# Kernel tuning notes

Measured on AMD Instinct MI355X. Metric: run time of the kernel, lower is better.

## Reference

```python
import jax, jax.numpy as jnp
import numpy as np

STATE_DIM = 8
SLOT_DIM = 128
B, T, K = 128, 6, 64


def _mlp(x, w1, b1, w2, b2):
    return jax.nn.relu(x @ w1 + b1) @ w2 + b2


def setup_inputs() -> dict:
    key = jax.random.key(0)
    ks = jax.random.split(key, 24)
    s = 0.02
    def w(k, shape):
        return jax.random.normal(k, shape, dtype=jnp.float32) * s
    D, H = STATE_DIM, SLOT_DIM
    return {
        "gt_states": jax.random.normal(ks[0], (B, T, K, D), dtype=jnp.float32),
        "rollout_steps": 5,
        "enc_w1": w(ks[1], (D, H)),  "enc_b1": jnp.zeros((H,), jnp.float32),
        "enc_w2": w(ks[2], (H, H)),  "enc_b2": jnp.zeros((H,), jnp.float32),
        "self_w1": w(ks[3], (H, H)), "self_b1": jnp.zeros((H,), jnp.float32),
        "self_w2": w(ks[4], (H, H)), "self_b2": jnp.zeros((H,), jnp.float32),
        "inter_w1": w(ks[5], (2 * H, H)), "inter_b1": jnp.zeros((H,), jnp.float32),
        "inter_w2": w(ks[6], (H, H)),     "inter_b2": jnp.zeros((H,), jnp.float32),
        "upd_w1": w(ks[7], (2 * H, H)), "upd_b1": jnp.zeros((H,), jnp.float32),
        "upd_w2": w(ks[8], (H, H)),     "upd_b2": jnp.zeros((H,), jnp.float32),
        "dec_w1": w(ks[9], (H, H)),  "dec_b1": jnp.zeros((H,), jnp.float32),
        "dec_w2": w(ks[10], (H, D)), "dec_b2": jnp.zeros((D,), jnp.float32),
    }


def reference(gt_states, rollout_steps, enc_w1, enc_b1, enc_w2, enc_b2,
              self_w1, self_b1, self_w2, self_b2,
              inter_w1, inter_b1, inter_w2, inter_b2,
              upd_w1, upd_b1, upd_w2, upd_b2,
              dec_w1, dec_b1, dec_w2, dec_b2):
    Tn = gt_states.shape[1]
    n_steps = min(Tn - 1, int(rollout_steps))
    H = enc_w1.shape[1]
    # split the concat-MLP first layer: cat([si, sj]) @ W1 == si @ W1a + sj @ W1b
    wi_a, wi_b = inter_w1[:H], inter_w1[H:]

    slots = _mlp(gt_states[:, 0], enc_w1, enc_b1, enc_w2, enc_b2)  # [B,K,H]
    preds = []
    for _ in range(n_steps):
        delta_self = _mlp(slots, self_w1, self_b1, self_w2, self_b2)  # [B,K,H]
        a = slots @ wi_a  # sender (i) contribution, [B,K,H]
        b = slots @ wi_b  # receiver (j) contribution, [B,K,H]
        # pairwise pre-activation [B,K(i),K(j),H]
        pre = a[:, :, None, :] + b[:, None, :, :] + inter_b1
        effects = jax.nn.relu(pre) @ inter_w2 + inter_b2  # [B,K,K,H]
        delta_inter = effects.mean(axis=1)  # mean over i -> [B,K,H]
        slots = _mlp(jnp.concatenate([delta_self, delta_inter], axis=-1),
                     upd_w1, upd_b1, upd_w2, upd_b2)
        pred = _mlp(slots, dec_w1, dec_b1, dec_w2, dec_b2)  # [B,K,D]
        preds.append(pred)
        slots = _mlp(pred, enc_w1, enc_b1, enc_w2, enc_b2)
    pred_states = jnp.stack(preds, axis=1)  # [B,n_steps,K,D]
    target_states = gt_states[:, 1:int(rollout_steps) + 1]
    return pred_states, target_states
```

## Files before the change

kernel.cpp:

```cpp
#include <hip/hip_runtime.h>

#define BB 128
#define TT 6
#define KK 64
#define DD 8
#define HH 128
#define NSTEP 5
#define LDP 136
#define PREDSZ (BB*NSTEP*KK*DD)

typedef unsigned short u16;
typedef unsigned int   u32;
typedef _Float16 f16;
typedef __attribute__((ext_vector_type(8))) _Float16 f16x8;
typedef __attribute__((ext_vector_type(4))) float f32x4;
typedef __attribute__((ext_vector_type(2))) unsigned int u32x2;
typedef __attribute__((ext_vector_type(4))) unsigned int u32x4;
typedef __attribute__((ext_vector_type(2))) _Float16 h2;

union h2u { u32 u; h2 h; };
union hu  { u16 u; f16 h; };

__device__ __forceinline__ u16 f2h_bits(float f){
  hu v; v.h = (f16)f; return v.u;
}
__device__ __forceinline__ u32 pk2(float x, float y){
  hu a, b; a.h = (f16)x; b.h = (f16)y;
  return (u32)a.u | ((u32)b.u << 16);
}
__device__ __forceinline__ h2 u2h(u32 x){ h2u t; t.u = x; return t.h; }
__device__ __forceinline__ u32 h2u_(h2 x){ h2u t; t.h = x; return t.u; }

#define O_EWA   0
#define O_EWB   16384
#define O_EWS   32768
#define O_SUIU  49152
#define O_UD    81920
#define O_DET   98304
#define O_DW2T  114688
#define BIASF   57856
#define O_XBUF  131072
#define O_FLAG  (O_XBUF + 128*2*2*4096)

template<bool RELU>
__device__ __forceinline__ void gemmH(const u16 (*A)[LDP], const u16* __restrict__ wt,
    float bias, u16 (*O)[LDP], int wn, int l15, int q, int n, int lane)
{
  f16x8 bf[4];
#pragma unroll
  for (int kc=0; kc<4; ++kc)
    bf[kc] = *(const f16x8*)(wt + (wn<<11) + (kc<<9) + (lane<<3));
#pragma unroll
  for (int mt=0; mt<2; ++mt){
    f32x4 acc = {0.f,0.f,0.f,0.f};
#pragma unroll
    for (int kc=0; kc<4; ++kc){
      f16x8 af = *(const f16x8*)&A[(mt<<4)+l15][(kc<<5)+(q<<3)];
      acc = __builtin_amdgcn_mfma_f32_16x16x32_f16(af, bf[kc], acc, 0,0,0);
    }
#pragma unroll
    for (int e=0; e<4; ++e){
      float v = acc[e] + bias;
      if (RELU) v = fmaxf(v, 0.f);
      O[(mt<<4)+(q<<2)+e][n] = f2h_bits(v);
    }
  }
}

__device__ __forceinline__ void gemm256H(const u16 (*A1)[LDP], const u16 (*A2)[LDP],
    const u16* __restrict__ wt, float bias, u16 (*O)[LDP], int wn, int l15, int q, int n, int lane)
{
  f16x8 bf[8];
#pragma unroll
  for (int kc=0; kc<8; ++kc)
    bf[kc] = *(const f16x8*)(wt + (wn<<12) + (kc<<9) + (lane<<3));
#pragma unroll
  for (int mt=0; mt<2; ++mt){
    f32x4 acc = {0.f,0.f,0.f,0.f};
#pragma unroll
    for (int kc=0; kc<8; ++kc){
      const u16 (*As)[LDP] = (kc<4) ? A1 : A2;
      f16x8 af = *(const f16x8*)&As[(mt<<4)+l15][((kc&3)<<5)+(q<<3)];
      acc = __builtin_amdgcn_mfma_f32_16x16x32_f16(af, bf[kc], acc, 0,0,0);
    }
#pragma unroll
    for (int e=0; e<4; ++e){
      float v = fmaxf(acc[e] + bias, 0.f);
      O[(mt<<4)+(q<<2)+e][n] = f2h_bits(v);
    }
  }
}

__device__ __forceinline__ void fusedS1I(const u16 (*P)[LDP], const u16* __restrict__ ws,
    float bAv, float bBv, float bSv,
    u16 (*Q)[LDP], u16 (*S)[LDP],
    int wn, int half, int l15, int q, int n, int lane)
{
  f16x8 fa[4], fb[4], fs[4];
#pragma unroll
  for (int kc=0; kc<4; ++kc){
    const int o = (wn<<11) + (kc<<9) + (lane<<3);
    fa[kc] = *(const f16x8*)(ws + O_EWA + o);
    fb[kc] = *(const f16x8*)(ws + O_EWB + o);
    fs[kc] = *(const f16x8*)(ws + O_EWS + o);
  }
  u32 aPk[4][2], bPk[4][2];
#pragma unroll
  for (int mt=0; mt<4; ++mt){
    f16x8 af[4];
#pragma unroll
    for (int kc=0; kc<4; ++kc)
      af[kc] = *(const f16x8*)&P[(mt<<4)+l15][(kc<<5)+(q<<3)];
    f32x4 aA = {0.f,0.f,0.f,0.f}, aB = {0.f,0.f,0.f,0.f};
#pragma unroll
    for (int kc=0; kc<4; ++kc){
      aA = __builtin_amdgcn_mfma_f32_16x16x32_f16(af[kc], fa[kc], aA, 0,0,0);
      aB = __builtin_amdgcn_mfma_f32_16x16x32_f16(af[kc], fb[kc], aB, 0,0,0);
    }
    aPk[mt][0] = pk2(aA[0]+bAv, aA[1]+bAv);
    aPk[mt][1] = pk2(aA[2]+bAv, aA[3]+bAv);
    bPk[mt][0] = pk2(aB[0]+bBv, aB[1]+bBv);
    bPk[mt][1] = pk2(aB[2]+bBv, aB[3]+bBv);
    if ((mt>>1) == half){
      f32x4 hA = {0.f,0.f,0.f,0.f};
#pragma unroll
      for (int kc=0; kc<4; ++kc)
        hA = __builtin_amdgcn_mfma_f32_16x16x32_f16(af[kc], fs[kc], hA, 0,0,0);
#pragma unroll
      for (int e=0; e<4; ++e)
        S[((mt&1)<<4)+(q<<2)+e][n] = f2h_bits(fmaxf(hA[e]+bSv, 0.f));
    }
  }

  const u32 b0 = bPk[(half<<1)][0],   b1 = bPk[(half<<1)][1];
  const u32 b2 = bPk[(half<<1)+1][0], b3 = bPk[(half<<1)+1][1];
  u32 jt[4][4];
#pragma unroll
  for (int qp=0; qp<4; ++qp){
    const int src = (qp<<4) + l15;
    jt[qp][0] = (u32)__shfl((int)b0, src);
    jt[qp][1] = (u32)__shfl((int)b1, src);
    jt[qp][2] = (u32)__shfl((int)b2, src);
    jt[qp][3] = (u32)__shfl((int)b3, src);
  }
  h2 z; z.x = (f16)0.f; z.y = (f16)0.f;
  h2 s[4][4];
#pragma unroll
  for (int qp=0; qp<4; ++qp)
#pragma unroll
    for (int X=0; X<4; ++X) s[qp][X] = z;
#pragma unroll
  for (int mt=0; mt<4; ++mt)
#pragma unroll
    for (int p=0; p<2; ++p){
      const u32 ap = aPk[mt][p];
      const h2 hl = u2h(__builtin_amdgcn_perm(ap, ap, 0x01000100));
      const h2 hh = u2h(__builtin_amdgcn_perm(ap, ap, 0x03020302));
#pragma unroll
      for (int qp=0; qp<4; ++qp)
#pragma unroll
        for (int X=0; X<4; ++X){
          const h2 bt = u2h(jt[qp][X]);
          s[qp][X] += __builtin_elementwise_max(hl + bt, z);
          s[qp][X] += __builtin_elementwise_max(hh + bt, z);
        }
    }
#pragma unroll
  for (int m=0; m<2; ++m){
    const int msk = 16 << m;
#pragma unroll
    for (int qp=0; qp<4; ++qp)
#pragma unroll
      for (int X=0; X<4; ++X)
        s[qp][X] += u2h((u32)__shfl_xor((int)h2u_(s[qp][X]), msk));
  }
#pragma unroll
  for (int qp=0; qp<4; ++qp) if (qp == q){
#pragma unroll
    for (int X=0; X<4; ++X){
      const int mh = X>>1, p = X&1;
      const int j = (mh<<4) + (qp<<2) + (p<<1);
      hu lo, hi; lo.h = s[qp][X].x; hi.h = s[qp][X].y;
      Q[j][n]   = lo.u;
      Q[j+1][n] = hi.u;
    }
  }
}

__device__ __forceinline__ void dec_out(const u16 (*S)[LDP], const u16* __restrict__ dwt,
    float db2v, float* __restrict__ out, int batch, int half, int t, int tid)
{
  const int r = tid>>3, d = tid&7;
  float acc = db2v;
#pragma unroll
  for (int c=0; c<16; ++c){
    f16x8 hv = *(const f16x8*)&S[r][c<<3];
    f16x8 wv = *(const f16x8*)(dwt + (d<<7) + (c<<3));
#pragma unroll
    for (int j=0; j<8; ++j)
      acc += (float)hv[j] * (float)wv[j];
  }
  out[(size_t)(batch*NSTEP + t)*(KK*DD) + ((half<<5)+r)*DD + d] = acc;
}

__device__ __forceinline__ void mlp_in8(const float* pred, const float* __restrict__ W,
    const float* __restrict__ bias, u16 (*O)[LDP], int tid)
{
  const int h = tid & 127, rg = tid >> 7;
  float wv[DD];
#pragma unroll
  for (int d=0; d<DD; ++d) wv[d] = W[d*HH + h];
  const float bv = bias[h];
  for (int rr=0; rr<16; ++rr){
    const int r = (rg<<4) + rr;
    float v = bv;
#pragma unroll
    for (int d=0; d<DD; ++d) v += pred[r*DD + d] * wv[d];
    O[r][h] = f2h_bits(fmaxf(v, 0.f));
  }
}

__global__ void prep_kernel(
    const float* __restrict__ ew1, const float* __restrict__ eb1,
    const float* __restrict__ ew2, const float* __restrict__ eb2,
    const float* __restrict__ sw1, const float* __restrict__ sb1,
    const float* __restrict__ sw2, const float* __restrict__ sb2,
    const float* __restrict__ iw1, const float* __restrict__ ib1,
    const float* __restrict__ iw2, const float* __restrict__ ib2,
    const float* __restrict__ uw1, const float* __restrict__ ub1,
    const float* __restrict__ uw2, const float* __restrict__ ub2,
    const float* __restrict__ dw1, const float* __restrict__ db1,
    const float* __restrict__ dw2, const float* __restrict__ db2,
    u16* __restrict__ ws)
{
  const int idx = blockIdx.x * 256 + threadIdx.x;
  if (idx < 512) ((u32*)(ws + O_FLAG))[idx] = 0;
  if (idx < 49152){
    const int mat = idx >> 14, r = idx & 16383;
    const int g = r >> 11, kc = (r >> 9) & 3, lane = (r >> 3) & 63, e = r & 7;
    const int k  = (kc<<5) + ((lane>>4)<<3) + e;
    const int nn = (g<<4) + (lane & 15);
    float v = 0.f;
    if (mat == 0){ for (int m=0; m<HH; ++m) v += ew2[k*HH+m] * iw1[m*HH+nn]; }
    else if (mat == 1){ for (int m=0; m<HH; ++m) v += ew2[k*HH+m] * iw1[(HH+m)*HH+nn]; }
    else { for (int m=0; m<HH; ++m) v += ew2[k*HH+m] * sw1[m*HH+nn]; }
    hu hb; hb.h = (f16)v; ws[idx] = hb.u;
  } else if (idx < 81920){
    const int r = idx - 49152;
    const int g = r >> 12, kc = (r >> 9) & 7, lane = (r >> 3) & 63, e = r & 7;
    const int k  = ((kc&3)<<5) + ((lane>>4)<<3) + e;
    const int nn = (g<<4) + (lane & 15);
    float v = 0.f;
    if (kc < 4){ for (int m=0; m<HH; ++m) v += sw2[k*HH+m] * uw1[m*HH+nn]; }
    else { for (int m=0; m<HH; ++m) v += iw2[k*HH+m] * uw1[(HH+m)*HH+nn]; v *= (1.f/64.f); }
    hu hb; hb.h = (f16)v; ws[idx] = hb.u;
  } else if (idx < 98304){
    const int r = idx - 81920;
    const int g = r >> 11, kc = (r >> 9) & 3, lane = (r >> 3) & 63, e = r & 7;
    const int k  = (kc<<5) + ((lane>>4)<<3) + e;
    const int nn = (g<<4) + (lane & 15);
    float v = 0.f;
    for (int m=0; m<HH; ++m) v += uw2[k*HH+m] * dw1[m*HH+nn];
    hu hb; hb.h = (f16)v; ws[idx] = hb.u;
  } else if (idx < 114688){
    const int r = idx - 98304;
    const int g = r >> 11, kc = (r >> 9) & 3, lane = (r >> 3) & 63, e = r & 7;
    const int k  = (kc<<5) + ((lane>>4)<<3) + e;
    const int nn = (g<<4) + (lane & 15);
    float v = 0.f;
#pragma unroll
    for (int d=0; d<DD; ++d) v += dw2[k*DD+d] * ew1[d*HH+nn];
    hu hb; hb.h = (f16)v; ws[idx] = hb.u;
  } else if (idx < 115712){
    const int r = idx - 114688, d = r >> 7, hcol = r & 127;
    hu hb; hb.h = (f16)dw2[hcol*DD + d]; ws[idx] = hb.u;
  } else if (idx < 116480){
    const int j = idx - 115712, which = j >> 7, nn = j & 127;
    float v = 0.f;
    switch (which){
      case 0: for (int m=0; m<HH; ++m) v += eb2[m] * iw1[m*HH+nn]; break;
      case 1: for (int m=0; m<HH; ++m) v += eb2[m] * iw1[(HH+m)*HH+nn]; v += ib1[nn]; break;
      case 2: for (int m=0; m<HH; ++m) v += eb2[m] * sw1[m*HH+nn]; v += sb1[nn]; break;
      case 3: for (int m=0; m<HH; ++m) v += sb2[m]*uw1[m*HH+nn] + ib2[m]*uw1[(HH+m)*HH+nn];
              v += ub1[nn]; break;
      case 4: for (int m=0; m<HH; ++m) v += ub2[m] * dw1[m*HH+nn]; v += db1[nn]; break;
      default:
#pragma unroll
        for (int d=0; d<DD; ++d) v += db2[d] * ew1[d*HH+nn];
        v += eb1[nn]; break;
    }
    ((float*)ws)[BIASF + j] = v;
  }
}

__global__ __launch_bounds__(512, 2) void rollout_kernel(
    const float* __restrict__ gt, const int* __restrict__ rollout,
    const float* __restrict__ ew1, const float* __restrict__ eb1,
    const float* __restrict__ db2,
    u16* __restrict__ ws, float* __restrict__ out)
{
  extern __shared__ u16 smem[];
  u16 (*P)[LDP] = (u16(*)[LDP])smem;
  u16 (*Q)[LDP] = (u16(*)[LDP])(smem + 64*LDP);
  u16 (*R)[LDP] = (u16(*)[LDP])(smem + 96*LDP);
  u16 (*S)[LDP] = (u16(*)[LDP])(smem + 128*LDP);
  float* predbuf = (float*)Q;

  const int tid = threadIdx.x, blk = blockIdx.x;
  const int batch = blk & 127, half = blk >> 7;
  const int w = tid >> 6, lane = tid & 63;
  const int l15 = lane & 15, q = lane >> 4;
  const int wn = w;
  const int n = (wn << 4) + l15;

  int ns = rollout[0];
  if (ns > TT-1) ns = TT-1;
  if (ns > NSTEP) ns = NSTEP;
  if (ns < 0) ns = 0;

  const float* bf32 = (const float*)ws;
  const float bAv  = bf32[BIASF + n];
  const float bBv  = bf32[BIASF + 128 + n];
  const float bSv  = bf32[BIASF + 256 + n];
  const float bUv  = bf32[BIASF + 384 + n];
  const float bUDv = bf32[BIASF + 512 + n];
  const float debv = bf32[BIASF + 640 + n];
  const float db2v = db2[tid & 7];

  u16* xbuf  = ws + O_XBUF;
  u32* flags = (u32*)(ws + O_FLAG);
  const int own  = (batch<<1) + half;
  const int prt  = (batch<<1) + (1-half);

  for (int i=tid; i<NSTEP*KK*DD/2; i+=512)
    out[PREDSZ + batch*(NSTEP*KK*DD) + half*(NSTEP*KK*DD/2) + i]
      = gt[(size_t)batch*(TT*KK*DD) + KK*DD + half*(NSTEP*KK*DD/2) + i];
  predbuf[tid] = gt[(size_t)batch*(TT*KK*DD) + tid];
  __syncthreads();
  mlp_in8(predbuf, ew1, eb1, P, tid);
  __syncthreads();

  for (int t=0; t<ns; ++t){
    fusedS1I(P, ws, bAv, bBv, bSv, Q, S, wn, half, l15, q, n, lane);
    __syncthreads();
    gemm256H(S, Q, ws+O_SUIU, bUv, R, wn, l15, q, n, lane);
    __syncthreads();
    gemmH<true>(R, ws+O_UD, bUDv, S, wn, l15, q, n, lane);
    __syncthreads();
    gemmH<true>(S, ws+O_DET, debv, P + (half<<5), wn, l15, q, n, lane);
    if (tid < 256) dec_out(S, ws+O_DW2T, db2v, out, batch, half, t, tid);
    __syncthreads();

    if (t < ns-1){
      const int par = t & 1;
      u16* ob = xbuf + (((own<<1)|par) << 12);
      {
        const int r = tid >> 4, c = (tid & 15) << 3;
        *(f16x8*)(ob + tid*8) = *(const f16x8*)&P[(half<<5)+r][c];
      }
      __syncthreads();
      if (tid == 0){
        __hip_atomic_store(&flags[(own<<1)|par], (u32)(t+1),
                           __ATOMIC_RELEASE, __HIP_MEMORY_SCOPE_AGENT);
        int guard = 0;
        while (__hip_atomic_load(&flags[(prt<<1)|par],
                 __ATOMIC_ACQUIRE, __HIP_MEMORY_SCOPE_AGENT) != (u32)(t+1)
               && guard < (1<<22)){
          ++guard;
          __builtin_amdgcn_s_sleep(1);
        }
      }
      __syncthreads();
      {
        const u16* pb = xbuf + (((prt<<1)|par) << 12);
        const int r = tid >> 4, c = (tid & 15) << 3;
        *(f16x8*)&P[((1-half)<<5)+r][c] = *(const f16x8*)(pb + tid*8);
      }
      __syncthreads();
    }
  }
}

extern "C" void kernel_launch(void* const* d_in, const int* in_sizes, int n_in,
                              void* d_out, int out_size, void* d_ws, size_t ws_size,
                              hipStream_t stream)
{
  const float* gt  = (const float*)d_in[0];
  const int*   rs  = (const int*)d_in[1];
  const float* ew1 = (const float*)d_in[2];
  const float* eb1 = (const float*)d_in[3];
  const float* ew2 = (const float*)d_in[4];
  const float* eb2 = (const float*)d_in[5];
  const float* sw1 = (const float*)d_in[6];
  const float* sb1 = (const float*)d_in[7];
  const float* sw2 = (const float*)d_in[8];
  const float* sb2 = (const float*)d_in[9];
  const float* iw1 = (const float*)d_in[10];
  const float* ib1 = (const float*)d_in[11];
  const float* iw2 = (const float*)d_in[12];
  const float* ib2 = (const float*)d_in[13];
  const float* uw1 = (const float*)d_in[14];
  const float* ub1 = (const float*)d_in[15];
  const float* uw2 = (const float*)d_in[16];
  const float* ub2 = (const float*)d_in[17];
  const float* dw1 = (const float*)d_in[18];
  const float* db1 = (const float*)d_in[19];
  const float* dw2 = (const float*)d_in[20];
  const float* db2 = (const float*)d_in[21];
  float* out = (float*)d_out;
  u16*   ws  = (u16*)d_ws;

  const int smem_bytes = 160 * LDP * (int)sizeof(u16);
  (void)hipFuncSetAttribute((const void*)rollout_kernel,
                            hipFuncAttributeMaxDynamicSharedMemorySize, smem_bytes);

  hipLaunchKernelGGL(prep_kernel, dim3(455), dim3(256), 0, stream,
                     ew1, eb1, ew2, eb2, sw1, sb1, sw2, sb2, iw1, ib1, iw2, ib2,
                     uw1, ub1, uw2, ub2, dw1, db1, dw2, db2, ws);
  hipLaunchKernelGGL(rollout_kernel, dim3(2*BB), dim3(512), smem_bytes, stream,
                     gt, rs, ew1, eb1, db2, ws, out);
}
```

Before: 198.3 us.

## Split each batch across four cooperating blocks instead of two

```diff
diff --git a/kernel.cpp b/kernel.cpp
--- a/kernel.cpp
+++ b/kernel.cpp
@@ -14,8 +14,6 @@
 typedef _Float16 f16;
 typedef __attribute__((ext_vector_type(8))) _Float16 f16x8;
 typedef __attribute__((ext_vector_type(4))) float f32x4;
-typedef __attribute__((ext_vector_type(2))) unsigned int u32x2;
-typedef __attribute__((ext_vector_type(4))) unsigned int u32x4;
 typedef __attribute__((ext_vector_type(2))) _Float16 h2;
 
 union h2u { u32 u; h2 h; };
@@ -40,129 +38,122 @@
 #define O_DW2T  114688
 #define BIASF   57856
 #define O_XBUF  131072
-#define O_FLAG  (O_XBUF + 128*2*2*4096)
+#define O_FLAG  (O_XBUF + 128*4*2*2048)
 
 template<bool RELU>
-__device__ __forceinline__ void gemmH(const u16 (*A)[LDP], const u16* __restrict__ wt,
+__device__ __forceinline__ void gemm16(const u16 (*A)[LDP], const u16* __restrict__ wt,
     float bias, u16 (*O)[LDP], int wn, int l15, int q, int n, int lane)
 {
   f16x8 bf[4];
 #pragma unroll
   for (int kc=0; kc<4; ++kc)
     bf[kc] = *(const f16x8*)(wt + (wn<<11) + (kc<<9) + (lane<<3));
-#pragma unroll
-  for (int mt=0; mt<2; ++mt){
-    f32x4 acc = {0.f,0.f,0.f,0.f};
-#pragma unroll
-    for (int kc=0; kc<4; ++kc){
-      f16x8 af = *(const f16x8*)&A[(mt<<4)+l15][(kc<<5)+(q<<3)];
-      acc = __builtin_amdgcn_mfma_f32_16x16x32_f16(af, bf[kc], acc, 0,0,0);
-    }
-#pragma unroll
-    for (int e=0; e<4; ++e){
-      float v = acc[e] + bias;
-      if (RELU) v = fmaxf(v, 0.f);
-      O[(mt<<4)+(q<<2)+e][n] = f2h_bits(v);
-    }
-  }
-}
-
-__device__ __forceinline__ void gemm256H(const u16 (*A1)[LDP], const u16 (*A2)[LDP],
+  f32x4 acc = {0.f,0.f,0.f,0.f};
+#pragma unroll
+  for (int kc=0; kc<4; ++kc){
+    f16x8 af = *(const f16x8*)&A[l15][(kc<<5)+(q<<3)];
+    acc = __builtin_amdgcn_mfma_f32_16x16x32_f16(af, bf[kc], acc, 0,0,0);
+  }
+#pragma unroll
+  for (int e=0; e<4; ++e){
+    float v = acc[e] + bias;
+    if (RELU) v = fmaxf(v, 0.f);
+    O[(q<<2)+e][n] = f2h_bits(v);
+  }
+}
+
+__device__ __forceinline__ void gemm256_16(const u16 (*A1)[LDP], const u16 (*A2)[LDP],
     const u16* __restrict__ wt, float bias, u16 (*O)[LDP], int wn, int l15, int q, int n, int lane)
 {
   f16x8 bf[8];
 #pragma unroll
   for (int kc=0; kc<8; ++kc)
     bf[kc] = *(const f16x8*)(wt + (wn<<12) + (kc<<9) + (lane<<3));
-#pragma unroll
-  for (int mt=0; mt<2; ++mt){
-    f32x4 acc = {0.f,0.f,0.f,0.f};
-#pragma unroll
-    for (int kc=0; kc<8; ++kc){
-      const u16 (*As)[LDP] = (kc<4) ? A1 : A2;
-      f16x8 af = *(const f16x8*)&As[(mt<<4)+l15][((kc&3)<<5)+(q<<3)];
-      acc = __builtin_amdgcn_mfma_f32_16x16x32_f16(af, bf[kc], acc, 0,0,0);
-    }
-#pragma unroll
-    for (int e=0; e<4; ++e){
-      float v = fmaxf(acc[e] + bias, 0.f);
-      O[(mt<<4)+(q<<2)+e][n] = f2h_bits(v);
-    }
+  f32x4 acc = {0.f,0.f,0.f,0.f};
+#pragma unroll
+  for (int kc=0; kc<8; ++kc){
+    const u16 (*As)[LDP] = (kc<4) ? A1 : A2;
+    f16x8 af = *(const f16x8*)&As[l15][((kc&3)<<5)+(q<<3)];
+    acc = __builtin_amdgcn_mfma_f32_16x16x32_f16(af, bf[kc], acc, 0,0,0);
+  }
+#pragma unroll
+  for (int e=0; e<4; ++e){
+    float v = fmaxf(acc[e] + bias, 0.f);
+    O[(q<<2)+e][n] = f2h_bits(v);
   }
 }
 
 __device__ __forceinline__ void fusedS1I(const u16 (*P)[LDP], const u16* __restrict__ ws,
     float bAv, float bBv, float bSv,
     u16 (*Q)[LDP], u16 (*S)[LDP],
-    int wn, int half, int l15, int q, int n, int lane)
-{
-  f16x8 fa[4], fb[4], fs[4];
-#pragma unroll
-  for (int kc=0; kc<4; ++kc){
-    const int o = (wn<<11) + (kc<<9) + (lane<<3);
-    fa[kc] = *(const f16x8*)(ws + O_EWA + o);
-    fb[kc] = *(const f16x8*)(ws + O_EWB + o);
-    fs[kc] = *(const f16x8*)(ws + O_EWS + o);
-  }
-  u32 aPk[4][2], bPk[4][2];
-#pragma unroll
-  for (int mt=0; mt<4; ++mt){
-    f16x8 af[4];
+    int wn, int qtr, int l15, int q, int n, int lane)
+{
+  u32 aPk[4][2];
+  {
+    f16x8 fa[4];
 #pragma unroll
     for (int kc=0; kc<4; ++kc)
-      af[kc] = *(const f16x8*)&P[(mt<<4)+l15][(kc<<5)+(q<<3)];
-    f32x4 aA = {0.f,0.f,0.f,0.f}, aB = {0.f,0.f,0.f,0.f};
+      fa[kc] = *(const f16x8*)(ws + O_EWA + (wn<<11) + (kc<<9) + (lane<<3));
+#pragma unroll
+    for (int mt=0; mt<4; ++mt){
+      f32x4 aA = {0.f,0.f,0.f,0.f};
+#pragma unroll
+      for (int kc=0; kc<4; ++kc){
+        f16x8 af = *(const f16x8*)&P[(mt<<4)+l15][(kc<<5)+(q<<3)];
+        aA = __builtin_amdgcn_mfma_f32_16x16x32_f16(af, fa[kc], aA, 0,0,0);
+      }
+      aPk[mt][0] = pk2(aA[0]+bAv, aA[1]+bAv);
+      aPk[mt][1] = pk2(aA[2]+bAv, aA[3]+bAv);
+    }
+  }
+  u32 bPk[2];
+  {
+    f16x8 fb[4], fs[4], af[4];
 #pragma unroll
     for (int kc=0; kc<4; ++kc){
-      aA = __builtin_amdgcn_mfma_f32_16x16x32_f16(af[kc], fa[kc], aA, 0,0,0);
+      const int o = (wn<<11) + (kc<<9) + (lane<<3);
+      fb[kc] = *(const f16x8*)(ws + O_EWB + o);
+      fs[kc] = *(const f16x8*)(ws + O_EWS + o);
+      af[kc] = *(const f16x8*)&P[(qtr<<4)+l15][(kc<<5)+(q<<3)];
+    }
+    f32x4 aB = {0.f,0.f,0.f,0.f}, aS = {0.f,0.f,0.f,0.f};
+#pragma unroll
+    for (int kc=0; kc<4; ++kc){
       aB = __builtin_amdgcn_mfma_f32_16x16x32_f16(af[kc], fb[kc], aB, 0,0,0);
-    }
-    aPk[mt][0] = pk2(aA[0]+bAv, aA[1]+bAv);
-    aPk[mt][1] = pk2(aA[2]+bAv, aA[3]+bAv);
-    bPk[mt][0] = pk2(aB[0]+bBv, aB[1]+bBv);
-    bPk[mt][1] = pk2(aB[2]+bBv, aB[3]+bBv);
-    if ((mt>>1) == half){
-      f32x4 hA = {0.f,0.f,0.f,0.f};
-#pragma unroll
-      for (int kc=0; kc<4; ++kc)
-        hA = __builtin_amdgcn_mfma_f32_16x16x32_f16(af[kc], fs[kc], hA, 0,0,0);
-#pragma unroll
-      for (int e=0; e<4; ++e)
-        S[((mt&1)<<4)+(q<<2)+e][n] = f2h_bits(fmaxf(hA[e]+bSv, 0.f));
-    }
-  }
-
-  const u32 b0 = bPk[(half<<1)][0],   b1 = bPk[(half<<1)][1];
-  const u32 b2 = bPk[(half<<1)+1][0], b3 = bPk[(half<<1)+1][1];
-  u32 jt[4][4];
+      aS = __builtin_amdgcn_mfma_f32_16x16x32_f16(af[kc], fs[kc], aS, 0,0,0);
+    }
+    bPk[0] = pk2(aB[0]+bBv, aB[1]+bBv);
+    bPk[1] = pk2(aB[2]+bBv, aB[3]+bBv);
+#pragma unroll
+    for (int e=0; e<4; ++e)
+      S[(q<<2)+e][n] = f2h_bits(fmaxf(aS[e]+bSv, 0.f));
+  }
+
+  u32 jt[4][2];
 #pragma unroll
   for (int qp=0; qp<4; ++qp){
     const int src = (qp<<4) + l15;
-    jt[qp][0] = (u32)__shfl((int)b0, src);
-    jt[qp][1] = (u32)__shfl((int)b1, src);
-    jt[qp][2] = (u32)__shfl((int)b2, src);
-    jt[qp][3] = (u32)__shfl((int)b3, src);
+    jt[qp][0] = (u32)__shfl((int)bPk[0], src);
+    jt[qp][1] = (u32)__shfl((int)bPk[1], src);
   }
   h2 z; z.x = (f16)0.f; z.y = (f16)0.f;
-  h2 s[4][4];
-#pragma unroll
-  for (int qp=0; qp<4; ++qp)
-#pragma unroll
-    for (int X=0; X<4; ++X) s[qp][X] = z;
+  h2 s[4][2];
+#pragma unroll
+  for (int qp=0; qp<4; ++qp){ s[qp][0] = z; s[qp][1] = z; }
 #pragma unroll
   for (int mt=0; mt<4; ++mt)
 #pragma unroll
-    for (int p=0; p<2; ++p){
-      const u32 ap = aPk[mt][p];
+    for (int pp=0; pp<2; ++pp){
+      const u32 ap = aPk[mt][pp];
       const h2 hl = u2h(__builtin_amdgcn_perm(ap, ap, 0x01000100));
       const h2 hh = u2h(__builtin_amdgcn_perm(ap, ap, 0x03020302));
 #pragma unroll
       for (int qp=0; qp<4; ++qp)
 #pragma unroll
-        for (int X=0; X<4; ++X){
-          const h2 bt = u2h(jt[qp][X]);
-          s[qp][X] += __builtin_elementwise_max(hl + bt, z);
-          s[qp][X] += __builtin_elementwise_max(hh + bt, z);
+        for (int p=0; p<2; ++p){
+          const h2 bt = u2h(jt[qp][p]);
+          s[qp][p] += __builtin_elementwise_max(hl + bt, z);
+          s[qp][p] += __builtin_elementwise_max(hh + bt, z);
         }
     }
 #pragma unroll
@@ -171,16 +162,15 @@
 #pragma unroll
     for (int qp=0; qp<4; ++qp)
 #pragma unroll
-      for (int X=0; X<4; ++X)
-        s[qp][X] += u2h((u32)__shfl_xor((int)h2u_(s[qp][X]), msk));
+      for (int p=0; p<2; ++p)
+        s[qp][p] += u2h((u32)__shfl_xor((int)h2u_(s[qp][p]), msk));
   }
 #pragma unroll
   for (int qp=0; qp<4; ++qp) if (qp == q){
 #pragma unroll
-    for (int X=0; X<4; ++X){
-      const int mh = X>>1, p = X&1;
-      const int j = (mh<<4) + (qp<<2) + (p<<1);
-      hu lo, hi; lo.h = s[qp][X].x; hi.h = s[qp][X].y;
+    for (int p=0; p<2; ++p){
+      const int j = (qp<<2) + (p<<1);
+      hu lo, hi; lo.h = s[qp][p].x; hi.h = s[qp][p].y;
       Q[j][n]   = lo.u;
       Q[j+1][n] = hi.u;
     }
@@ -188,7 +178,7 @@
 }
 
 __device__ __forceinline__ void dec_out(const u16 (*S)[LDP], const u16* __restrict__ dwt,
-    float db2v, float* __restrict__ out, int batch, int half, int t, int tid)
+    float db2v, float* __restrict__ out, int batch, int qtr, int t, int tid)
 {
   const int r = tid>>3, d = tid&7;
   float acc = db2v;
@@ -200,7 +190,7 @@
     for (int j=0; j<8; ++j)
       acc += (float)hv[j] * (float)wv[j];
   }
-  out[(size_t)(batch*NSTEP + t)*(KK*DD) + ((half<<5)+r)*DD + d] = acc;
+  out[(size_t)(batch*NSTEP + t)*(KK*DD) + ((qtr<<4)+r)*DD + d] = acc;
 }
 
 __device__ __forceinline__ void mlp_in8(const float* pred, const float* __restrict__ W,
@@ -234,7 +224,7 @@
     u16* __restrict__ ws)
 {
   const int idx = blockIdx.x * 256 + threadIdx.x;
-  if (idx < 512) ((u32*)(ws + O_FLAG))[idx] = 0;
+  if (idx < 1024) ((u32*)(ws + O_FLAG))[idx] = 0;
   if (idx < 49152){
     const int mat = idx >> 14, r = idx & 16383;
     const int g = r >> 11, kc = (r >> 9) & 3, lane = (r >> 3) & 63, e = r & 7;
@@ -302,12 +292,12 @@
   extern __shared__ u16 smem[];
   u16 (*P)[LDP] = (u16(*)[LDP])smem;
   u16 (*Q)[LDP] = (u16(*)[LDP])(smem + 64*LDP);
-  u16 (*R)[LDP] = (u16(*)[LDP])(smem + 96*LDP);
-  u16 (*S)[LDP] = (u16(*)[LDP])(smem + 128*LDP);
+  u16 (*R)[LDP] = (u16(*)[LDP])(smem + 80*LDP);
+  u16 (*S)[LDP] = (u16(*)[LDP])(smem + 96*LDP);
   float* predbuf = (float*)Q;
 
   const int tid = threadIdx.x, blk = blockIdx.x;
-  const int batch = blk & 127, half = blk >> 7;
+  const int batch = blk & 127, qtr = blk >> 7;
   const int w = tid >> 6, lane = tid & 63;
   const int l15 = lane & 15, q = lane >> 4;
   const int wn = w;
@@ -329,52 +319,70 @@
 
   u16* xbuf  = ws + O_XBUF;
   u32* flags = (u32*)(ws + O_FLAG);
-  const int own  = (batch<<1) + half;
-  const int prt  = (batch<<1) + (1-half);
-
-  for (int i=tid; i<NSTEP*KK*DD/2; i+=512)
-    out[PREDSZ + batch*(NSTEP*KK*DD) + half*(NSTEP*KK*DD/2) + i]
-      = gt[(size_t)batch*(TT*KK*DD) + KK*DD + half*(NSTEP*KK*DD/2) + i];
+
+  for (int i = tid; i < (NSTEP*KK*DD/4); i += 512)
+    out[PREDSZ + batch*(NSTEP*KK*DD) + qtr*(NSTEP*KK*DD/4) + i]
+      = gt[(size_t)batch*(TT*KK*DD) + KK*DD + qtr*(NSTEP*KK*DD/4) + i];
   predbuf[tid] = gt[(size_t)batch*(TT*KK*DD) + tid];
   __syncthreads();
   mlp_in8(predbuf, ew1, eb1, P, tid);
   __syncthreads();
 
   for (int t=0; t<ns; ++t){
-    fusedS1I(P, ws, bAv, bBv, bSv, Q, S, wn, half, l15, q, n, lane);
+    fusedS1I(P, ws, bAv, bBv, bSv, Q, S, wn, qtr, l15, q, n, lane);
     __syncthreads();
-    gemm256H(S, Q, ws+O_SUIU, bUv, R, wn, l15, q, n, lane);
+    gemm256_16(S, Q, ws+O_SUIU, bUv, R, wn, l15, q, n, lane);
     __syncthreads();
-    gemmH<true>(R, ws+O_UD, bUDv, S, wn, l15, q, n, lane);
+    gemm16<true>(R, ws+O_UD, bUDv, S, wn, l15, q, n, lane);
     __syncthreads();
-    gemmH<true>(S, ws+O_DET, debv, P + (half<<5), wn, l15, q, n, lane);
-    if (tid < 256) dec_out(S, ws+O_DW2T, db2v, out, batch, half, t, tid);
+    {
+      f16x8 bfw[4];
+#pragma unroll
+      for (int kc=0; kc<4; ++kc)
+        bfw[kc] = *(const f16x8*)(ws + O_DET + (wn<<11) + (kc<<9) + (lane<<3));
+      f32x4 acc = {0.f,0.f,0.f,0.f};
+#pragma unroll
+      for (int kc=0; kc<4; ++kc){
+        f16x8 af = *(const f16x8*)&S[l15][(kc<<5)+(q<<3)];
+        acc = __builtin_amdgcn_mfma_f32_16x16x32_f16(af, bfw[kc], acc, 0,0,0);
+      }
+      const int par = t & 1;
+      u16* ob = xbuf + ((((batch<<2)|qtr)<<1|par)<<11);
+      const bool exch = (t < ns-1);
+#pragma unroll
+      for (int e=0; e<4; ++e){
+        const u16 bits = f2h_bits(fmaxf(acc[e]+debv, 0.f));
+        P[(qtr<<4)+(q<<2)+e][n] = bits;
+        if (exch) ob[(((q<<2)+e)<<7) | n] = bits;
+      }
+    }
+    if (tid < 128) dec_out(S, ws+O_DW2T, db2v, out, batch, qtr, t, tid);
     __syncthreads();
 
     if (t < ns-1){
       const int par = t & 1;
-      u16* ob = xbuf + (((own<<1)|par) << 12);
-      {
-        const int r = tid >> 4, c = (tid & 15) << 3;
-        *(f16x8*)(ob + tid*8) = *(const f16x8*)&P[(half<<5)+r][c];
-      }
-      __syncthreads();
       if (tid == 0){
-        __hip_atomic_store(&flags[(own<<1)|par], (u32)(t+1),
+        __hip_atomic_store(&flags[((batch<<2)|qtr)<<1|par], (u32)(t+1),
                            __ATOMIC_RELEASE, __HIP_MEMORY_SCOPE_AGENT);
-        int guard = 0;
-        while (__hip_atomic_load(&flags[(prt<<1)|par],
-                 __ATOMIC_ACQUIRE, __HIP_MEMORY_SCOPE_AGENT) != (u32)(t+1)
-               && guard < (1<<22)){
-          ++guard;
-          __builtin_amdgcn_s_sleep(1);
+#pragma unroll
+        for (int qq=0; qq<4; ++qq) if (qq != qtr){
+          int guard = 0;
+          while (__hip_atomic_load(&flags[((batch<<2)|qq)<<1|par],
+                   __ATOMIC_ACQUIRE, __HIP_MEMORY_SCOPE_AGENT) != (u32)(t+1)
+                 && guard < (1<<22)){
+            ++guard;
+            __builtin_amdgcn_s_sleep(1);
+          }
         }
       }
       __syncthreads();
-      {
-        const u16* pb = xbuf + (((prt<<1)|par) << 12);
+      if (tid < 256){
         const int r = tid >> 4, c = (tid & 15) << 3;
-        *(f16x8*)&P[((1-half)<<5)+r][c] = *(const f16x8*)(pb + tid*8);
+#pragma unroll
+        for (int qq=0; qq<4; ++qq) if (qq != qtr){
+          const u16* pb = xbuf + ((((batch<<2)|qq)<<1|par)<<11);
+          *(f16x8*)&P[(qq<<4)+r][c] = *(const f16x8*)(pb + (r<<7) + c);
+        }
       }
       __syncthreads();
     }
@@ -410,13 +418,13 @@
   float* out = (float*)d_out;
   u16*   ws  = (u16*)d_ws;
 
-  const int smem_bytes = 160 * LDP * (int)sizeof(u16);
+  const int smem_bytes = 112 * LDP * (int)sizeof(u16);
   (void)hipFuncSetAttribute((const void*)rollout_kernel,
                             hipFuncAttributeMaxDynamicSharedMemorySize, smem_bytes);
 
   hipLaunchKernelGGL(prep_kernel, dim3(455), dim3(256), 0, stream,
                      ew1, eb1, ew2, eb2, sw1, sb1, sw2, sb2, iw1, ib1, iw2, ib2,
                      uw1, ub1, uw2, ub2, dw1, db1, dw2, db2, ws);
-  hipLaunchKernelGGL(rollout_kernel, dim3(2*BB), dim3(512), smem_bytes, stream,
+  hipLaunchKernelGGL(rollout_kernel, dim3(4*BB), dim3(512), smem_bytes, stream,
                      gt, rs, ew1, eb1, db2, ws, out);
 }
```

After: 297.8 us. +50.2%, slower.
